# Kernel tuning notes

Measured on AMD Instinct MI355X. Metric: run time of the kernel, lower is better.

## Reference

```python
import jax, jax.numpy as jnp
import numpy as np

N = 100000        # nodes
E = 3200000       # directed edges (already includes both directions per the repo)
F_IN = 256
HID = 16
C = 40


def setup_inputs() -> dict:
    key = jax.random.key(0)
    k = jax.random.split(key, 5)
    x = jax.random.normal(k[0], (N, F_IN), dtype=jnp.float32)
    edge_index = jax.random.randint(k[1], (2, E), 0, N, dtype=jnp.int64)
    W1 = jax.random.normal(k[2], (F_IN, HID), dtype=jnp.float32) * (1.0 / np.sqrt(F_IN))
    b1 = jnp.zeros((HID,), jnp.float32)
    W2 = jax.random.normal(k[3], (HID, C), dtype=jnp.float32) * (1.0 / np.sqrt(HID))
    b2 = jnp.zeros((C,), jnp.float32)
    return {"x": x, "edge_index": edge_index, "W1": W1, "b1": b1, "W2": W2, "b2": b2}


def reference(x, edge_index, W1, b1, W2, b2):
    n = x.shape[0]
    # GCNConv: add self-loops, symmetric degree normalization (shared by both layers)
    loop = jnp.arange(n, dtype=edge_index.dtype)
    src = jnp.concatenate([edge_index[0], loop])
    dst = jnp.concatenate([edge_index[1], loop])
    deg = jax.ops.segment_sum(jnp.ones_like(dst, x.dtype), dst, num_segments=n)
    dinv = jnp.where(deg > 0, jax.lax.rsqrt(deg), 0.0)
    norm = dinv[src] * dinv[dst]  # [E+N]

    def gcn(h, W, b):
        h = h @ W  # transform first (PyG order), keeps edge messages low-dim
        msg = h[src] * norm[:, None]
        return jax.ops.segment_sum(msg, dst, num_segments=n) + b

    h = jax.nn.relu(gcn(x, W1, b1))
    # dropout is identity in eval mode (training=False)
    logits = gcn(h, W2, b2)
    return jax.nn.log_softmax(logits, axis=1)
```

## Files before the change

kernel.cpp:

```cpp
#include <hip/hip_runtime.h>
#include <hip/hip_bf16.h>


#define BSH 8
#define BCAP 9216
#define MAXB 512
#define OVF_CAP 8192
#define EPB 4096

typedef __attribute__((ext_vector_type(8))) short bf16x8;
typedef __attribute__((ext_vector_type(4))) short bf16x4;
typedef __attribute__((ext_vector_type(4))) float f32x4;

__device__ __forceinline__ short f2b(float f) {
    __hip_bfloat16 h = __float2bfloat16(f);
    return *reinterpret_cast<short*>(&h);
}
__device__ __forceinline__ float b2f(short s) {
    return __uint_as_float(((unsigned int)(unsigned short)s) << 16);
}

__global__ __launch_bounds__(512) void binA(
        const int* __restrict__ src, const int* __restrict__ dst,
        int* __restrict__ gcur, int* __restrict__ padded,
        int2* __restrict__ ovf, int* __restrict__ ovf_cnt,
        int* __restrict__ deg, int E) {
    __shared__ int hist[MAXB], gb[MAXB];
    int tid = threadIdx.x;
    int e0 = blockIdx.x * EPB;
    int e1 = min(e0 + EPB, E);
    if (tid < MAXB) hist[tid] = 0;
    __syncthreads();
    int rs[8], rd[8];
#pragma unroll
    for (int u = 0; u < 8; ++u) {
        int i = e0 + tid + u * 512;
        if (i < e1) {
            rd[u] = dst[i];
            rs[u] = src[i];
            atomicAdd(&hist[rd[u] >> BSH], 1);
        }
    }
    __syncthreads();
    if (tid < MAXB) {
        int h = hist[tid];
        gb[tid] = h ? atomicAdd(&gcur[tid], h) : 0;
        hist[tid] = 0;
    }
    __syncthreads();
#pragma unroll
    for (int u = 0; u < 8; ++u) {
        int i = e0 + tid + u * 512;
        if (i < e1) {
            int s = rs[u], d = rd[u];
            int b = d >> BSH;
            int r = atomicAdd(&hist[b], 1);
            int off = gb[b] + r;
            if (off < BCAP) {
                padded[b * BCAP + off] = (s << BSH) | (d & ((1 << BSH) - 1));
            } else {
                int k = atomicAdd(ovf_cnt, 1);
                if (k < OVF_CAP) ovf[k] = make_int2(s, d);
                atomicAdd(&deg[d], 1);
            }
        }
    }
}

__global__ __launch_bounds__(1024) void binB(
        const int* __restrict__ gcur, int* __restrict__ padded,
        int2* __restrict__ og, int* __restrict__ deg, int n) {
    __shared__ int bins[256], scanb[256], sA[256];
    __shared__ int sorted[BCAP];
    int k = blockIdx.x, tid = threadIdx.x;
    int base = k * BCAP;
    int cnt = gcur[k];
    if (cnt > BCAP) cnt = BCAP;
    if (cnt < 0) cnt = 0;
    if (tid < 256) bins[tid] = 0;
    __syncthreads();
    for (int i = tid; i < cnt; i += 1024)
        atomicAdd(&bins[padded[base + i] & 255], 1);
    __syncthreads();
    if (tid < 256) sA[tid] = bins[tid];
    __syncthreads();
    for (int d = 1; d < 256; d <<= 1) {
        int v = 0, a = 0;
        if (tid < 256) {
            v = sA[tid];
            a = (tid >= d) ? sA[tid - d] : 0;
        }
        __syncthreads();
        if (tid < 256) sA[tid] = v + a;
        __syncthreads();
    }
    if (tid < 256) {
        int excl = sA[tid] - bins[tid];
        scanb[tid] = excl;
        int node = (k << BSH) + tid;
        if (node < n) {
            og[node] = make_int2(base + excl, bins[tid]);
            atomicAdd(&deg[node], bins[tid]);
        }
        bins[tid] = 0;
    }
    __syncthreads();
    for (int i = tid; i < cnt; i += 1024) {
        int v = padded[base + i];
        int lo = v & 255;
        int r = atomicAdd(&bins[lo], 1);
        sorted[scanb[lo] + r] = v >> BSH;
    }
    __syncthreads();
    for (int i = tid; i < cnt; i += 1024) padded[base + i] = sorted[i];
}

__global__ __launch_bounds__(512) void gemm1_mfma(
        const float* __restrict__ x, const float* __restrict__ W1,
        const int* __restrict__ deg, float* __restrict__ dinv,
        short* __restrict__ t1b, int n) {
    __shared__ __align__(16) short xs[128 * 264];
    __shared__ short w1s[256 * 16];
    int tid = threadIdx.x;
    int base = blockIdx.x * 128;
    int rows = n - base; if (rows > 128) rows = 128;

    for (int i = tid; i < 4096; i += 512) w1s[i] = f2b(W1[i]);
    for (int i = tid; i < 8192; i += 512) {
        int r = i >> 6, c = i & 63;
        if (r < rows) {
            float4 v = ((const float4*)(x + (size_t)(base + r) * 256))[c];
            short4 b;
            b.x = f2b(v.x); b.y = f2b(v.y); b.z = f2b(v.z); b.w = f2b(v.w);
            *(short4*)&xs[r * 264 + c * 4] = b;
        }
    }
    __syncthreads();

    int lane = tid & 63, wave = tid >> 6;
    int q = lane >> 4, m = lane & 15;

    bf16x8 bfrag[8];
#pragma unroll
    for (int t = 0; t < 8; ++t)
#pragma unroll
        for (int j = 0; j < 8; ++j)
            bfrag[t][j] = w1s[(t * 32 + q * 8 + j) * 16 + m];

    f32x4 acc = {0.f, 0.f, 0.f, 0.f};
    int arow = wave * 16 + m;
#pragma unroll
    for (int t = 0; t < 8; ++t) {
        bf16x8 a = *(const bf16x8*)&xs[arow * 264 + t * 32 + q * 8];
        acc = __builtin_amdgcn_mfma_f32_16x16x32_bf16(a, bfrag[t], acc, 0, 0, 0);
    }
#pragma unroll
    for (int r = 0; r < 4; ++r) {
        int node = base + wave * 16 + q * 4 + r;
        if (node < n) {
            float di = rsqrtf((float)deg[node] + 1.0f);
            t1b[(size_t)node * 16 + m] = f2b(acc[r] * di);
            if (m == 0) dinv[node] = di;
        }
    }
}

template <int PHASE>
__global__ __launch_bounds__(256) void agg_k(
        const int2* __restrict__ og, const int* __restrict__ padded,
        const short* __restrict__ feat,
        short* __restrict__ Hout, const float* __restrict__ dinv,
        const float* __restrict__ b1,
        const float* __restrict__ W2, const float* __restrict__ b2,
        float* __restrict__ out, int n) {
    __shared__ float W2s[640];
    __shared__ float b2s[40];
    __shared__ float sAcc[64][17];
    int tid = threadIdx.x;
    if (PHASE == 1) {
        for (int i = tid; i < 640; i += 256) W2s[i] = W2[i];
        if (tid < 40) b2s[tid] = b2[tid];
        __syncthreads();
    }
    int nl   = tid >> 2;
    int node = blockIdx.x * 64 + nl;
    int q    = tid & 3;
    bool live = node < n;
    const bf16x4* f4 = (const bf16x4*)feat;
    float acc[4] = {0.f, 0.f, 0.f, 0.f};
    int b = 0, c = 0;
    if (live) {
        bf16x4 sv = f4[(size_t)node * 4 + q];
        acc[0] = b2f(sv[0]); acc[1] = b2f(sv[1]);
        acc[2] = b2f(sv[2]); acc[3] = b2f(sv[3]);
        int2 o = og[node]; b = o.x; c = o.y;
    }
    int j = 0;
    for (; j + 4 <= c; j += 4) {
        int s0 = padded[b + j],     s1 = padded[b + j + 1];
        int s2 = padded[b + j + 2], s3 = padded[b + j + 3];
        bf16x4 v0 = f4[(size_t)s0 * 4 + q];
        bf16x4 v1 = f4[(size_t)s1 * 4 + q];
        bf16x4 v2 = f4[(size_t)s2 * 4 + q];
        bf16x4 v3 = f4[(size_t)s3 * 4 + q];
#pragma unroll
        for (int h = 0; h < 4; ++h)
            acc[h] += (b2f(v0[h]) + b2f(v1[h])) + (b2f(v2[h]) + b2f(v3[h]));
    }
    for (; j < c; ++j) {
        bf16x4 v = f4[(size_t)padded[b + j] * 4 + q];
#pragma unroll
        for (int h = 0; h < 4; ++h) acc[h] += b2f(v[h]);
    }

    if (PHASE == 0) {
        if (live) {
            float di = dinv[node];
            float4 bb = ((const float4*)b1)[q];
            bf16x4 o4_;
            o4_[0] = f2b(fmaxf(bb.x + di * acc[0], 0.f) * di);
            o4_[1] = f2b(fmaxf(bb.y + di * acc[1], 0.f) * di);
            o4_[2] = f2b(fmaxf(bb.z + di * acc[2], 0.f) * di);
            o4_[3] = f2b(fmaxf(bb.w + di * acc[3], 0.f) * di);
            ((bf16x4*)Hout)[(size_t)node * 4 + q] = o4_;
        }
    } else {
        float di = live ? dinv[node] : 0.f;
#pragma unroll
        for (int h = 0; h < 4; ++h) sAcc[nl][q * 4 + h] = di * acc[h];
        __syncthreads();
        float gf[16];
#pragma unroll
        for (int k = 0; k < 16; ++k) gf[k] = sAcc[nl][k];
        float lg[10];
        float mx = -1e30f;
#pragma unroll
        for (int jj = 0; jj < 10; ++jj) {
            int col = q * 10 + jj;
            float a = b2s[col];
#pragma unroll
            for (int k = 0; k < 16; ++k) a += gf[k] * W2s[k * 40 + col];
            lg[jj] = a;
            mx = fmaxf(mx, a);
        }
        mx = fmaxf(mx, __shfl_xor(mx, 1));
        mx = fmaxf(mx, __shfl_xor(mx, 2));
        float sum = 0.f;
#pragma unroll
        for (int jj = 0; jj < 10; ++jj) sum += __expf(lg[jj] - mx);
        sum += __shfl_xor(sum, 1);
        sum += __shfl_xor(sum, 2);
        float lse = mx + logf(sum);
        if (live) {
            float2* o2 = (float2*)(out + (size_t)node * 40 + q * 10);
#pragma unroll
            for (int jj = 0; jj < 5; ++jj)
                o2[jj] = make_float2(lg[2 * jj] - lse, lg[2 * jj + 1] - lse);
        }
    }
}

extern "C" void kernel_launch(void* const* d_in, const int* in_sizes, int n_in,
                              void* d_out, int out_size, void* d_ws, size_t ws_size,
                              hipStream_t stream) {
    const float* x  = (const float*)d_in[0];
    const int*   ei = (const int*)d_in[1];
    const float* W1 = (const float*)d_in[2];
    const float* b1 = (const float*)d_in[3];
    const float* W2 = (const float*)d_in[4];
    const float* b2 = (const float*)d_in[5];

    int n = in_sizes[0] / 256;
    int E = in_sizes[1] / 2;
    const int* srcp = ei;
    const int* dstp = ei + E;

    int nbuckets = (n + 255) >> BSH;

    int2*  og      = (int2*)d_ws;
    int*   deg     = (int*)d_ws + 2 * (size_t)n;
    int*   gcur    = deg + n;
    int*   ovf_cnt = gcur + MAXB;
    float* dinv    = (float*)(ovf_cnt + 16);
    int2*  ovf     = (int2*)(dinv + n);
    short* t1b     = (short*)(ovf + OVF_CAP);
    short* hdb     = t1b + 16 * (size_t)n;
    int*   padded  = (int*)(hdb + 16 * (size_t)n);
    float* out     = (float*)d_out;

    hipMemsetAsync(deg, 0, (size_t)(n + MAXB + 16) * sizeof(int), stream);
    binA      <<<(E + EPB - 1) / EPB, 512, 0, stream>>>(srcp, dstp, gcur, padded,
                                                        ovf, ovf_cnt, deg, E);
    binB      <<<nbuckets, 1024, 0, stream>>>(gcur, padded, og, deg, n);
    gemm1_mfma<<<(n + 127) / 128, 512, 0, stream>>>(x, W1, deg, dinv, t1b, n);
    agg_k<0>  <<<(n + 63) / 64, 256, 0, stream>>>(og, padded, t1b, hdb, dinv,
                                                  b1, nullptr, nullptr, nullptr, n);
    agg_k<1>  <<<(n + 63) / 64, 256, 0, stream>>>(og, padded, hdb, nullptr, dinv,
                                                  nullptr, W2, b2, out, n);
    final_dummy:;
}
```

Baseline: 301.0 us.

## Replace per-node CSR sort with bucket-local LDS atomic aggregation

Buckets shrink from 256 to 128 destination nodes. The in-bucket counting sort (binB) is replaced by a lightweight degree-count kernel. Each aggregation kernel now processes one bucket per block, gathering source features and accumulating into a shared-memory accumulator with LDS float atomics, then applying the epilogue per node. This removes the sort pass and its extra global writes and reads, at the cost of LDS atomic contention. It also makes the summation order nondeterministic.

```diff
diff --git a/kernel.cpp b/kernel.cpp
--- a/kernel.cpp
+++ b/kernel.cpp
@@ -2,9 +2,10 @@
 #include <hip/hip_bf16.h>
 
 
-#define BSH 8
-#define BCAP 9216
-#define MAXB 512
+#define BSH 7
+#define NPB 128
+#define BCAP 4736
+#define MAXB 1024
 #define OVF_CAP 8192
 #define EPB 4096
 
@@ -29,7 +30,7 @@
     int tid = threadIdx.x;
     int e0 = blockIdx.x * EPB;
     int e1 = min(e0 + EPB, E);
-    if (tid < MAXB) hist[tid] = 0;
+    for (int b = tid; b < MAXB; b += 512) hist[b] = 0;
     __syncthreads();
     int rs[8], rd[8];
 #pragma unroll
@@ -42,10 +43,10 @@
         }
     }
     __syncthreads();
-    if (tid < MAXB) {
-        int h = hist[tid];
-        gb[tid] = h ? atomicAdd(&gcur[tid], h) : 0;
-        hist[tid] = 0;
+    for (int b = tid; b < MAXB; b += 512) {
+        int h = hist[b];
+        gb[b] = h ? atomicAdd(&gcur[b], h) : 0;
+        hist[b] = 0;
     }
     __syncthreads();
 #pragma unroll
@@ -57,7 +58,7 @@
             int r = atomicAdd(&hist[b], 1);
             int off = gb[b] + r;
             if (off < BCAP) {
-                padded[b * BCAP + off] = (s << BSH) | (d & ((1 << BSH) - 1));
+                padded[b * BCAP + off] = (s << BSH) | (d & (NPB - 1));
             } else {
                 int k = atomicAdd(ovf_cnt, 1);
                 if (k < OVF_CAP) ovf[k] = make_int2(s, d);
@@ -67,52 +68,22 @@
     }
 }
 
-__global__ __launch_bounds__(1024) void binB(
-        const int* __restrict__ gcur, int* __restrict__ padded,
-        int2* __restrict__ og, int* __restrict__ deg, int n) {
-    __shared__ int bins[256], scanb[256], sA[256];
-    __shared__ int sorted[BCAP];
+__global__ __launch_bounds__(512) void degB(
+        const int* __restrict__ gcur, const int* __restrict__ padded,
+        int* __restrict__ deg, int n) {
+    __shared__ int bins[NPB];
     int k = blockIdx.x, tid = threadIdx.x;
+    if (tid < NPB) bins[tid] = 0;
+    __syncthreads();
     int base = k * BCAP;
-    int cnt = gcur[k];
-    if (cnt > BCAP) cnt = BCAP;
-    if (cnt < 0) cnt = 0;
-    if (tid < 256) bins[tid] = 0;
-    __syncthreads();
-    for (int i = tid; i < cnt; i += 1024)
-        atomicAdd(&bins[padded[base + i] & 255], 1);
-    __syncthreads();
-    if (tid < 256) sA[tid] = bins[tid];
-    __syncthreads();
-    for (int d = 1; d < 256; d <<= 1) {
-        int v = 0, a = 0;
-        if (tid < 256) {
-            v = sA[tid];
-            a = (tid >= d) ? sA[tid - d] : 0;
-        }
-        __syncthreads();
-        if (tid < 256) sA[tid] = v + a;
-        __syncthreads();
-    }
-    if (tid < 256) {
-        int excl = sA[tid] - bins[tid];
-        scanb[tid] = excl;
+    int cnt = min(gcur[k], BCAP);
+    for (int i = tid; i < cnt; i += 512)
+        atomicAdd(&bins[padded[base + i] & (NPB - 1)], 1);
+    __syncthreads();
+    if (tid < NPB) {
         int node = (k << BSH) + tid;
-        if (node < n) {
-            og[node] = make_int2(base + excl, bins[tid]);
-            atomicAdd(&deg[node], bins[tid]);
-        }
-        bins[tid] = 0;
-    }
-    __syncthreads();
-    for (int i = tid; i < cnt; i += 1024) {
-        int v = padded[base + i];
-        int lo = v & 255;
-        int r = atomicAdd(&bins[lo], 1);
-        sorted[scanb[lo] + r] = v >> BSH;
-    }
-    __syncthreads();
-    for (int i = tid; i < cnt; i += 1024) padded[base + i] = sorted[i];
+        if (node < n) atomicAdd(&deg[node], bins[tid]);
+    }
 }
 
 __global__ __launch_bounds__(512) void gemm1_mfma(
@@ -166,96 +137,95 @@
 }
 
 template <int PHASE>
-__global__ __launch_bounds__(256) void agg_k(
-        const int2* __restrict__ og, const int* __restrict__ padded,
+__global__ __launch_bounds__(512) void aggB(
+        const int* __restrict__ gcur, const int* __restrict__ padded,
         const short* __restrict__ feat,
         short* __restrict__ Hout, const float* __restrict__ dinv,
         const float* __restrict__ b1,
         const float* __restrict__ W2, const float* __restrict__ b2,
         float* __restrict__ out, int n) {
+    __shared__ float acc[NPB][17];
     __shared__ float W2s[640];
     __shared__ float b2s[40];
-    __shared__ float sAcc[64][17];
-    int tid = threadIdx.x;
+    int tid = threadIdx.x, k = blockIdx.x;
     if (PHASE == 1) {
-        for (int i = tid; i < 640; i += 256) W2s[i] = W2[i];
+        for (int i = tid; i < 640; i += 512) W2s[i] = W2[i];
         if (tid < 40) b2s[tid] = b2[tid];
-        __syncthreads();
-    }
-    int nl   = tid >> 2;
-    int node = blockIdx.x * 64 + nl;
-    int q    = tid & 3;
-    bool live = node < n;
+    }
+    for (int i = tid; i < NPB * 17; i += 512) ((float*)acc)[i] = 0.f;
+    __syncthreads();
+
+    int base = k * BCAP;
+    int cnt = min(gcur[k], BCAP);
     const bf16x4* f4 = (const bf16x4*)feat;
-    float acc[4] = {0.f, 0.f, 0.f, 0.f};
-    int b = 0, c = 0;
-    if (live) {
-        bf16x4 sv = f4[(size_t)node * 4 + q];
-        acc[0] = b2f(sv[0]); acc[1] = b2f(sv[1]);
-        acc[2] = b2f(sv[2]); acc[3] = b2f(sv[3]);
-        int2 o = og[node]; b = o.x; c = o.y;
-    }
-    int j = 0;
-    for (; j + 4 <= c; j += 4) {
-        int s0 = padded[b + j],     s1 = padded[b + j + 1];
-        int s2 = padded[b + j + 2], s3 = padded[b + j + 3];
-        bf16x4 v0 = f4[(size_t)s0 * 4 + q];
-        bf16x4 v1 = f4[(size_t)s1 * 4 + q];
-        bf16x4 v2 = f4[(size_t)s2 * 4 + q];
-        bf16x4 v3 = f4[(size_t)s3 * 4 + q];
-#pragma unroll
-        for (int h = 0; h < 4; ++h)
-            acc[h] += (b2f(v0[h]) + b2f(v1[h])) + (b2f(v2[h]) + b2f(v3[h]));
-    }
-    for (; j < c; ++j) {
-        bf16x4 v = f4[(size_t)padded[b + j] * 4 + q];
-#pragma unroll
-        for (int h = 0; h < 4; ++h) acc[h] += b2f(v[h]);
-    }
+    int q = tid & 3;
+    for (int i = tid >> 2; i < cnt; i += 128) {
+        int v = padded[base + i];
+        int s = v >> BSH;
+        int dl = v & (NPB - 1);
+        bf16x4 g = f4[(size_t)s * 4 + q];
+        atomicAdd(&acc[dl][q * 4 + 0], b2f(g[0]));
+        atomicAdd(&acc[dl][q * 4 + 1], b2f(g[1]));
+        atomicAdd(&acc[dl][q * 4 + 2], b2f(g[2]));
+        atomicAdd(&acc[dl][q * 4 + 3], b2f(g[3]));
+    }
+    __syncthreads();
 
     if (PHASE == 0) {
-        if (live) {
-            float di = dinv[node];
-            float4 bb = ((const float4*)b1)[q];
-            bf16x4 o4_;
-            o4_[0] = f2b(fmaxf(bb.x + di * acc[0], 0.f) * di);
-            o4_[1] = f2b(fmaxf(bb.y + di * acc[1], 0.f) * di);
-            o4_[2] = f2b(fmaxf(bb.z + di * acc[2], 0.f) * di);
-            o4_[3] = f2b(fmaxf(bb.w + di * acc[3], 0.f) * di);
-            ((bf16x4*)Hout)[(size_t)node * 4 + q] = o4_;
+        if (tid < 256) {
+            int nl = tid & (NPB - 1), half = tid >> 7;
+            int node = (k << BSH) + nl;
+            if (node < n) {
+                float di = dinv[node];
+                bf16x8 sv = ((const bf16x8*)feat)[(size_t)node * 2 + half];
+                float4 bA = ((const float4*)b1)[half * 2];
+                float4 bB = ((const float4*)b1)[half * 2 + 1];
+                float bb[8] = {bA.x, bA.y, bA.z, bA.w, bB.x, bB.y, bB.z, bB.w};
+                bf16x8 o8;
+#pragma unroll
+                for (int h = 0; h < 8; ++h) {
+                    float sfull = b2f(sv[h]) + acc[nl][half * 8 + h];
+                    o8[h] = f2b(fmaxf(bb[h] + di * sfull, 0.f) * di);
+                }
+                ((bf16x8*)Hout)[(size_t)node * 2 + half] = o8;
+            }
         }
     } else {
-        float di = live ? dinv[node] : 0.f;
-#pragma unroll
-        for (int h = 0; h < 4; ++h) sAcc[nl][q * 4 + h] = di * acc[h];
-        __syncthreads();
-        float gf[16];
-#pragma unroll
-        for (int k = 0; k < 16; ++k) gf[k] = sAcc[nl][k];
-        float lg[10];
-        float mx = -1e30f;
-#pragma unroll
-        for (int jj = 0; jj < 10; ++jj) {
-            int col = q * 10 + jj;
-            float a = b2s[col];
-#pragma unroll
-            for (int k = 0; k < 16; ++k) a += gf[k] * W2s[k * 40 + col];
-            lg[jj] = a;
-            mx = fmaxf(mx, a);
-        }
-        mx = fmaxf(mx, __shfl_xor(mx, 1));
-        mx = fmaxf(mx, __shfl_xor(mx, 2));
-        float sum = 0.f;
-#pragma unroll
-        for (int jj = 0; jj < 10; ++jj) sum += __expf(lg[jj] - mx);
-        sum += __shfl_xor(sum, 1);
-        sum += __shfl_xor(sum, 2);
-        float lse = mx + logf(sum);
-        if (live) {
-            float2* o2 = (float2*)(out + (size_t)node * 40 + q * 10);
-#pragma unroll
-            for (int jj = 0; jj < 5; ++jj)
-                o2[jj] = make_float2(lg[2 * jj] - lse, lg[2 * jj + 1] - lse);
+        if (tid < 256) {
+            int nl = tid >> 1, c20 = (tid & 1) * 20;
+            int node = (k << BSH) + nl;
+            if (node < n) {
+                float di = dinv[node];
+                bf16x8 s0 = ((const bf16x8*)feat)[(size_t)node * 2];
+                bf16x8 s1 = ((const bf16x8*)feat)[(size_t)node * 2 + 1];
+                float g[16];
+#pragma unroll
+                for (int h = 0; h < 8; ++h) {
+                    g[h]     = di * (b2f(s0[h]) + acc[nl][h]);
+                    g[h + 8] = di * (b2f(s1[h]) + acc[nl][h + 8]);
+                }
+                float lg[20], mx = -1e30f;
+#pragma unroll
+                for (int jj = 0; jj < 20; ++jj) {
+                    int col = c20 + jj;
+                    float a = b2s[col];
+#pragma unroll
+                    for (int kk = 0; kk < 16; ++kk) a += g[kk] * W2s[kk * 40 + col];
+                    lg[jj] = a;
+                    mx = fmaxf(mx, a);
+                }
+                mx = fmaxf(mx, __shfl_xor(mx, 1));
+                float sum = 0.f;
+#pragma unroll
+                for (int jj = 0; jj < 20; ++jj) sum += __expf(lg[jj] - mx);
+                sum += __shfl_xor(sum, 1);
+                float lse = mx + logf(sum);
+                float4* o4 = (float4*)(out + (size_t)node * 40 + c20);
+#pragma unroll
+                for (int j = 0; j < 5; ++j)
+                    o4[j] = make_float4(lg[4 * j] - lse, lg[4 * j + 1] - lse,
+                                        lg[4 * j + 2] - lse, lg[4 * j + 3] - lse);
+            }
         }
     }
 }
@@ -275,10 +245,9 @@
     const int* srcp = ei;
     const int* dstp = ei + E;
 
-    int nbuckets = (n + 255) >> BSH;
-
-    int2*  og      = (int2*)d_ws;
-    int*   deg     = (int*)d_ws + 2 * (size_t)n;
+    int nbuckets = (n + NPB - 1) >> BSH;
+
+    int*   deg     = (int*)d_ws;
     int*   gcur    = deg + n;
     int*   ovf_cnt = gcur + MAXB;
     float* dinv    = (float*)(ovf_cnt + 16);
@@ -289,13 +258,12 @@
     float* out     = (float*)d_out;
 
     hipMemsetAsync(deg, 0, (size_t)(n + MAXB + 16) * sizeof(int), stream);
-    binA      <<<(E + EPB - 1) / EPB, 512, 0, stream>>>(srcp, dstp, gcur, padded,
-                                                        ovf, ovf_cnt, deg, E);
-    binB      <<<nbuckets, 1024, 0, stream>>>(gcur, padded, og, deg, n);
+    binA    <<<(E + EPB - 1) / EPB, 512, 0, stream>>>(srcp, dstp, gcur, padded,
+                                                      ovf, ovf_cnt, deg, E);
+    degB    <<<nbuckets, 512, 0, stream>>>(gcur, padded, deg, n);
     gemm1_mfma<<<(n + 127) / 128, 512, 0, stream>>>(x, W1, deg, dinv, t1b, n);
-    agg_k<0>  <<<(n + 63) / 64, 256, 0, stream>>>(og, padded, t1b, hdb, dinv,
-                                                  b1, nullptr, nullptr, nullptr, n);
-    agg_k<1>  <<<(n + 63) / 64, 256, 0, stream>>>(og, padded, hdb, nullptr, dinv,
-                                                  nullptr, W2, b2, out, n);
-    final_dummy:;
-}
+    aggB<0> <<<nbuckets, 512, 0, stream>>>(gcur, padded, t1b, hdb, dinv,
+                                           b1, nullptr, nullptr, nullptr, n);
+    aggB<1> <<<nbuckets, 512, 0, stream>>>(gcur, padded, hdb, nullptr, dinv,
+                                           nullptr, W2, b2, out, n);
+}
```

After: 902.6 us. +199.8%, slower.
